# Performance work log

Measured on AMD Instinct MI355X. Metric: run time of the kernel, lower is better.

## Reference

```python
import jax, jax.numpy as jnp
import numpy as np

N = 131072; E = 1048576; B = 1024
FIN = 128; H = 128; K = 30; C1 = 16; KERN = 5
D = 3 * H                      # 384 = hidden*num_layers
POOL_LEN = (K - KERN + 1) // 2 # 13
EPS = 1e-5


def setup_inputs() -> dict:
    key = jax.random.key(0)
    ks = jax.random.split(key, 12)
    w = lambda k, shape, s=0.05: (jax.random.normal(k, shape, jnp.float32) * s)
    z = jax.random.randint(ks[0], (N,), 0, FIN, dtype=jnp.int32)
    edge_index = jax.random.randint(ks[1], (2, E), 0, N, dtype=jnp.int32)
    batch = jnp.sort(jax.random.randint(ks[2], (N,), 0, B, dtype=jnp.int32))
    return dict(
        z=z, edge_index=edge_index, batch=batch,
        W0=w(ks[3], (FIN, H)), b0=jnp.zeros((H,), jnp.float32),
        W1=w(ks[4], (H, H)),   b1=jnp.zeros((H,), jnp.float32),
        W2=w(ks[5], (H, H)),   b2=jnp.zeros((H,), jnp.float32),
        Wc1=w(ks[6], (C1, D)), bc1=jnp.zeros((C1,), jnp.float32),
        Wc2=w(ks[7], (2 * C1, C1, KERN)), bc2=jnp.zeros((2 * C1,), jnp.float32),
        g1=jnp.ones((C1,), jnp.float32),  be1=jnp.zeros((C1,), jnp.float32),
        g2=jnp.ones((2 * C1,), jnp.float32), be2=jnp.zeros((2 * C1,), jnp.float32),
        Wl1=w(ks[8], (128, 2 * C1 * POOL_LEN)), bl1=jnp.zeros((128,), jnp.float32),
        Wl2=w(ks[9], (1, 128)), bl2=jnp.zeros((1,), jnp.float32),
        rm1=jnp.zeros((C1,), jnp.float32), rv1=jnp.ones((C1,), jnp.float32),
        rm2=jnp.zeros((2 * C1,), jnp.float32), rv2=jnp.ones((2 * C1,), jnp.float32),
    )


def _bn(h, g, be, rm, rv):
    # eval-mode BatchNorm1d over channel axis 1 of [B, C, L]
    scale = (g * jax.lax.rsqrt(rv + EPS))[None, :, None]
    return (h - rm[None, :, None]) * scale + be[None, :, None]


def _forward(z, edge_index, batch, W0, b0, W1, b1, W2, b2, Wc1, bc1, Wc2, bc2,
             g1, be1, g2, be2, Wl1, bl1, Wl2, bl2, rm1, rv1, rm2, rv2):
    # --- GCN normalization with self-loops (PyG gcn_norm) ---
    loops = jnp.arange(N)
    row = jnp.concatenate([edge_index[0], loops])  # source
    col = jnp.concatenate([edge_index[1], loops])  # target (aggregation)
    deg = jax.ops.segment_sum(jnp.ones(E + N, jnp.float32), col, num_segments=N)
    dis = jax.lax.rsqrt(deg)  # deg >= 1 thanks to self-loops
    norm = dis[row] * dis[col]

    def gcn(x, W, b):
        msg = (x @ W)[row] * norm[:, None]              # [E+N, H]
        return jax.ops.segment_sum(msg, col, num_segments=N) + b

    x = jax.nn.one_hot(z, FIN, dtype=jnp.float32)       # [N, FIN]
    xs = []
    for W, b in ((W0, b0), (W1, b1), (W2, b2)):
        x = jnp.tanh(gcn(x, W, b))
        xs.append(x)
    x = jnp.concatenate(xs, axis=-1)                    # [N, D]

    # --- global_sort_pool: per graph, sort by last channel desc, keep top-k, zero-pad ---
    order = jnp.lexsort((-x[:, -1], batch))             # batch asc, last-channel desc
    xb, bs = x[order], batch[order]
    counts = jax.ops.segment_sum(jnp.ones(N, jnp.int32), batch, num_segments=B)
    starts = jnp.cumsum(counts) - counts
    rank = jnp.arange(N) - starts[bs]                   # within-graph rank
    dest = jnp.where(rank < K, rank, K)                 # overflow bucket at K
    pooled = jnp.zeros((B, K + 1, D), jnp.float32).at[bs, dest].set(xb)[:, :K]  # [B,K,D]

    # --- conv1d_1 (kernel=stride=D) == dense over the D channels of each kept node ---
    h = jnp.einsum('bkd,cd->bck', pooled, Wc1) + bc1[None, :, None]  # [B,C1,K]
    h = _bn(jax.nn.relu(h), g1, be1, rm1, rv1)
    # --- conv1d_2 ---
    h = jax.lax.conv_general_dilated(h, Wc2, (1,), 'VALID',
                                     dimension_numbers=('NCH', 'OIH', 'NCH'))
    h = h + bc2[None, :, None]                          # [B,2C1,K-KERN+1]
    h = _bn(jax.nn.relu(h), g2, be2, rm2, rv2)
    # --- maxpool(2,2), flatten, dense head (dropout is identity in eval) ---
    h = h.reshape(B, 2 * C1, POOL_LEN, 2).max(-1)
    h = jax.nn.relu(h.reshape(B, -1) @ Wl1.T + bl1)
    return (h @ Wl2.T + bl2).reshape(-1)                # [B]


def reference(z, edge_index, batch, W0, b0, W1, b1, W2, b2, Wc1, bc1, Wc2, bc2,
              g1, be1, g2, be2, Wl1, bl1, Wl2, bl2, rm1, rv1, rm2, rv2):
    return _forward(z, edge_index, batch, W0, b0, W1, b1, W2, b2, Wc1, bc1, Wc2, bc2,
                    g1, be1, g2, be2, Wl1, bl1, Wl2, bl2, rm1, rv1, rm2, rv2)
```

## Files before the change

### kernel.cpp

```cpp
#include <hip/hip_runtime.h>
#include <math.h>

constexpr int HD = 128;
constexpr int DD = 384;
constexpr int KK = 30;
constexpr int C1N = 16;
constexpr int C2N = 32;
constexpr int KERN5 = 5;
constexpr int CONVL = 26;
constexpr int PL = 13;
constexpr int FLAT = 416;

__global__ void deg_kernel(const int* __restrict__ col, int* __restrict__ cnt, int E) {
  int e = blockIdx.x * blockDim.x + threadIdx.x;
  if (e < E) atomicAdd(&cnt[col[e]], 1);
}

__global__ void scan1_kernel(const int* __restrict__ cnt, int* __restrict__ bsum, int N) {
  __shared__ int red[256];
  int t = threadIdx.x, b = blockIdx.x;
  int base = b * 1024 + t * 4;
  int s = 0;
#pragma unroll
  for (int j = 0; j < 4; ++j) { int idx = base + j; if (idx < N) s += cnt[idx]; }
  red[t] = s;
  __syncthreads();
  for (int o = 128; o > 0; o >>= 1) { if (t < o) red[t] += red[t + o]; __syncthreads(); }
  if (t == 0) bsum[b] = red[0];
}

__global__ void scan2_kernel(int* __restrict__ bsum, int nb) {
  __shared__ int s[1024];
  int t = threadIdx.x;
  int v = (t < nb) ? bsum[t] : 0;
  s[t] = v;
  __syncthreads();
  for (int o = 1; o < 1024; o <<= 1) {
    int u = (t >= o) ? s[t - o] : 0;
    __syncthreads();
    s[t] += u;
    __syncthreads();
  }
  if (t < nb) bsum[t] = s[t] - v;
}

__global__ void scan3_kernel(const int* __restrict__ cnt, const int* __restrict__ bsum,
                             int* __restrict__ offsets, float* __restrict__ dis, int N) {
  __shared__ int red[256];
  int t = threadIdx.x, b = blockIdx.x;
  int base = b * 1024 + t * 4;
  int v[4]; int s = 0;
#pragma unroll
  for (int j = 0; j < 4; ++j) { int idx = base + j; v[j] = (idx < N) ? cnt[idx] : 0; s += v[j]; }
  red[t] = s;
  __syncthreads();
  for (int o = 1; o < 256; o <<= 1) {
    int u = (t >= o) ? red[t - o] : 0;
    __syncthreads();
    red[t] += u;
    __syncthreads();
  }
  int run = bsum[b] + red[t] - s;
#pragma unroll
  for (int j = 0; j < 4; ++j) {
    int idx = base + j;
    if (idx < N) {
      offsets[idx] = run;
      run += v[j];
      dis[idx] = 1.0f / sqrtf((float)(v[j] + 1));
      if (idx == N - 1) offsets[N] = run;
    }
  }
}

__global__ void fill_kernel(const int* __restrict__ row, const int* __restrict__ col,
                            const int* __restrict__ offsets, int* __restrict__ cursor,
                            int* __restrict__ csr_src, int E) {
  int e = blockIdx.x * blockDim.x + threadIdx.x;
  if (e < E) {
    int c = col[e];
    int p = offsets[c] + atomicAdd(&cursor[c], 1);
    csr_src[p] = row[e];
  }
}

__global__ __launch_bounds__(256) void agg0_kernel(
    const int* __restrict__ z, const int* __restrict__ offsets,
    const int* __restrict__ csr_src, const float* __restrict__ dis,
    const float* __restrict__ W0, const float* __restrict__ b0,
    float* __restrict__ x1, int N) {
  int hw = (blockIdx.x * blockDim.x + threadIdx.x) >> 5;
  int lane = threadIdx.x & 31;
  if (hw >= N) return;
  int i = hw;
  int c0 = lane * 4;
  float di = dis[i];
  int beg = offsets[i], end = offsets[i + 1];
  float ax = 0.f, ay = 0.f, az = 0.f, aw = 0.f;
  int e = beg;
  for (; e + 8 <= end; e += 8) {
    int s0 = csr_src[e],     s1 = csr_src[e + 1], s2 = csr_src[e + 2], s3 = csr_src[e + 3];
    int s4 = csr_src[e + 4], s5 = csr_src[e + 5], s6 = csr_src[e + 6], s7 = csr_src[e + 7];
    float w0 = dis[s0], w1 = dis[s1], w2 = dis[s2], w3 = dis[s3];
    float w4 = dis[s4], w5 = dis[s5], w6 = dis[s6], w7 = dis[s7];
    const float4 y0 = *(const float4*)(W0 + (size_t)z[s0] * HD + c0);
    const float4 y1 = *(const float4*)(W0 + (size_t)z[s1] * HD + c0);
    const float4 y2 = *(const float4*)(W0 + (size_t)z[s2] * HD + c0);
    const float4 y3 = *(const float4*)(W0 + (size_t)z[s3] * HD + c0);
    const float4 y4 = *(const float4*)(W0 + (size_t)z[s4] * HD + c0);
    const float4 y5 = *(const float4*)(W0 + (size_t)z[s5] * HD + c0);
    const float4 y6 = *(const float4*)(W0 + (size_t)z[s6] * HD + c0);
    const float4 y7 = *(const float4*)(W0 + (size_t)z[s7] * HD + c0);
    ax = fmaf(w0, y0.x, fmaf(w1, y1.x, fmaf(w2, y2.x, fmaf(w3, y3.x, ax))));
    ay = fmaf(w0, y0.y, fmaf(w1, y1.y, fmaf(w2, y2.y, fmaf(w3, y3.y, ay))));
    az = fmaf(w0, y0.z, fmaf(w1, y1.z, fmaf(w2, y2.z, fmaf(w3, y3.z, az))));
    aw = fmaf(w0, y0.w, fmaf(w1, y1.w, fmaf(w2, y2.w, fmaf(w3, y3.w, aw))));
    ax = fmaf(w4, y4.x, fmaf(w5, y5.x, fmaf(w6, y6.x, fmaf(w7, y7.x, ax))));
    ay = fmaf(w4, y4.y, fmaf(w5, y5.y, fmaf(w6, y6.y, fmaf(w7, y7.y, ay))));
    az = fmaf(w4, y4.z, fmaf(w5, y5.z, fmaf(w6, y6.z, fmaf(w7, y7.z, az))));
    aw = fmaf(w4, y4.w, fmaf(w5, y5.w, fmaf(w6, y6.w, fmaf(w7, y7.w, aw))));
  }
  for (; e + 4 <= end; e += 4) {
    int s0 = csr_src[e], s1 = csr_src[e + 1], s2 = csr_src[e + 2], s3 = csr_src[e + 3];
    float w0 = dis[s0], w1 = dis[s1], w2 = dis[s2], w3 = dis[s3];
    const float4 y0 = *(const float4*)(W0 + (size_t)z[s0] * HD + c0);
    const float4 y1 = *(const float4*)(W0 + (size_t)z[s1] * HD + c0);
    const float4 y2 = *(const float4*)(W0 + (size_t)z[s2] * HD + c0);
    const float4 y3 = *(const float4*)(W0 + (size_t)z[s3] * HD + c0);
    ax = fmaf(w0, y0.x, fmaf(w1, y1.x, fmaf(w2, y2.x, fmaf(w3, y3.x, ax))));
    ay = fmaf(w0, y0.y, fmaf(w1, y1.y, fmaf(w2, y2.y, fmaf(w3, y3.y, ay))));
    az = fmaf(w0, y0.z, fmaf(w1, y1.z, fmaf(w2, y2.z, fmaf(w3, y3.z, az))));
    aw = fmaf(w0, y0.w, fmaf(w1, y1.w, fmaf(w2, y2.w, fmaf(w3, y3.w, aw))));
  }
  for (; e < end; ++e) {
    int s = csr_src[e];
    float w = dis[s];
    const float4 ys = *(const float4*)(W0 + (size_t)z[s] * HD + c0);
    ax = fmaf(w, ys.x, ax);
    ay = fmaf(w, ys.y, ay);
    az = fmaf(w, ys.z, az);
    aw = fmaf(w, ys.w, aw);
  }
  const float4 yi = *(const float4*)(W0 + (size_t)z[i] * HD + c0);
  const float4 bb = *(const float4*)(b0 + c0);
  float inv = di * di;
  float4 o = make_float4(tanhf(di * ax + inv * yi.x + bb.x),
                         tanhf(di * ay + inv * yi.y + bb.y),
                         tanhf(di * az + inv * yi.z + bb.z),
                         tanhf(di * aw + inv * yi.w + bb.w));
  *(float4*)(x1 + (size_t)i * HD + c0) = o;
}

__global__ __launch_bounds__(256) void agg_kernel(
    const float* __restrict__ x, const int* __restrict__ offsets,
    const int* __restrict__ csr_src, const float* __restrict__ dis,
    float* __restrict__ T, int N) {
  int hw = (blockIdx.x * blockDim.x + threadIdx.x) >> 5;
  int lane = threadIdx.x & 31;
  if (hw >= N) return;
  int i = hw;
  int c0 = lane * 4;
  float di = dis[i];
  int beg = offsets[i], end = offsets[i + 1];
  float ax = 0.f, ay = 0.f, az = 0.f, aw = 0.f;
  int e = beg;
  for (; e + 8 <= end; e += 8) {
    int s0 = csr_src[e],     s1 = csr_src[e + 1], s2 = csr_src[e + 2], s3 = csr_src[e + 3];
    int s4 = csr_src[e + 4], s5 = csr_src[e + 5], s6 = csr_src[e + 6], s7 = csr_src[e + 7];
    float w0 = dis[s0], w1 = dis[s1], w2 = dis[s2], w3 = dis[s3];
    float w4 = dis[s4], w5 = dis[s5], w6 = dis[s6], w7 = dis[s7];
    const float4 y0 = *(const float4*)(x + (size_t)s0 * HD + c0);
    const float4 y1 = *(const float4*)(x + (size_t)s1 * HD + c0);
    const float4 y2 = *(const float4*)(x + (size_t)s2 * HD + c0);
    const float4 y3 = *(const float4*)(x + (size_t)s3 * HD + c0);
    const float4 y4 = *(const float4*)(x + (size_t)s4 * HD + c0);
    const float4 y5 = *(const float4*)(x + (size_t)s5 * HD + c0);
    const float4 y6 = *(const float4*)(x + (size_t)s6 * HD + c0);
    const float4 y7 = *(const float4*)(x + (size_t)s7 * HD + c0);
    ax = fmaf(w0, y0.x, fmaf(w1, y1.x, fmaf(w2, y2.x, fmaf(w3, y3.x, ax))));
    ay = fmaf(w0, y0.y, fmaf(w1, y1.y, fmaf(w2, y2.y, fmaf(w3, y3.y, ay))));
    az = fmaf(w0, y0.z, fmaf(w1, y1.z, fmaf(w2, y2.z, fmaf(w3, y3.z, az))));
    aw = fmaf(w0, y0.w, fmaf(w1, y1.w, fmaf(w2, y2.w, fmaf(w3, y3.w, aw))));
    ax = fmaf(w4, y4.x, fmaf(w5, y5.x, fmaf(w6, y6.x, fmaf(w7, y7.x, ax))));
    ay = fmaf(w4, y4.y, fmaf(w5, y5.y, fmaf(w6, y6.y, fmaf(w7, y7.y, ay))));
    az = fmaf(w4, y4.z, fmaf(w5, y5.z, fmaf(w6, y6.z, fmaf(w7, y7.z, az))));
    aw = fmaf(w4, y4.w, fmaf(w5, y5.w, fmaf(w6, y6.w, fmaf(w7, y7.w, aw))));
  }
  for (; e + 4 <= end; e += 4) {
    int s0 = csr_src[e], s1 = csr_src[e + 1], s2 = csr_src[e + 2], s3 = csr_src[e + 3];
    float w0 = dis[s0], w1 = dis[s1], w2 = dis[s2], w3 = dis[s3];
    const float4 y0 = *(const float4*)(x + (size_t)s0 * HD + c0);
    const float4 y1 = *(const float4*)(x + (size_t)s1 * HD + c0);
    const float4 y2 = *(const float4*)(x + (size_t)s2 * HD + c0);
    const float4 y3 = *(const float4*)(x + (size_t)s3 * HD + c0);
    ax = fmaf(w0, y0.x, fmaf(w1, y1.x, fmaf(w2, y2.x, fmaf(w3, y3.x, ax))));
    ay = fmaf(w0, y0.y, fmaf(w1, y1.y, fmaf(w2, y2.y, fmaf(w3, y3.y, ay))));
    az = fmaf(w0, y0.z, fmaf(w1, y1.z, fmaf(w2, y2.z, fmaf(w3, y3.z, az))));
    aw = fmaf(w0, y0.w, fmaf(w1, y1.w, fmaf(w2, y2.w, fmaf(w3, y3.w, aw))));
  }
  for (; e < end; ++e) {
    int s = csr_src[e];
    float w = dis[s];
    const float4 ys = *(const float4*)(x + (size_t)s * HD + c0);
    ax = fmaf(w, ys.x, ax);
    ay = fmaf(w, ys.y, ay);
    az = fmaf(w, ys.z, az);
    aw = fmaf(w, ys.w, aw);
  }
  const float4 xi = *(const float4*)(x + (size_t)i * HD + c0);
  float inv = di * di;
  float4 o = make_float4(di * ax + inv * xi.x, di * ay + inv * xi.y,
                         di * az + inv * xi.z, di * aw + inv * xi.w);
  *(float4*)(T + (size_t)i * HD + c0) = o;
}

__global__ __launch_bounds__(512) void gemm_kernel(
    float* __restrict__ T, const float* __restrict__ W, const float* __restrict__ b, int N) {
  __shared__ float Xs[128][33];
  __shared__ float Ws[32][128];
  int t = threadIdx.x;
  int r0 = blockIdx.x * 128;
  int ty = t >> 4, tx = t & 15;
  int R0 = ty * 4;
  float acc[4][8];
#pragma unroll
  for (int a = 0; a < 4; ++a)
#pragma unroll
    for (int c = 0; c < 8; ++c) acc[a][c] = 0.f;

  for (int kb = 0; kb < 128; kb += 32) {
    __syncthreads();
    for (int l = t; l < 1024; l += 512) {
      int r = l >> 3, c4 = (l & 7) << 2;
      float4 v = *(const float4*)(T + (size_t)(r0 + r) * HD + kb + c4);
      Xs[r][c4] = v.x; Xs[r][c4 + 1] = v.y; Xs[r][c4 + 2] = v.z; Xs[r][c4 + 3] = v.w;
    }
    for (int l = t; l < 1024; l += 512) {
      int k = l >> 5, c4 = (l & 31) << 2;
      *(float4*)(&Ws[k][c4]) = *(const float4*)(W + (size_t)(kb + k) * HD + c4);
    }
    __syncthreads();
#pragma unroll
    for (int k = 0; k < 32; ++k) {
      float a[4];
#pragma unroll
      for (int ri = 0; ri < 4; ++ri) a[ri] = Xs[R0 + ri][k];
      float4 blo = *(const float4*)(&Ws[k][tx * 4]);
      float4 bhi = *(const float4*)(&Ws[k][64 + tx * 4]);
      float bb[8] = {blo.x, blo.y, blo.z, blo.w, bhi.x, bhi.y, bhi.z, bhi.w};
#pragma unroll
      for (int ri = 0; ri < 4; ++ri)
#pragma unroll
        for (int ci = 0; ci < 8; ++ci)
          acc[ri][ci] = fmaf(a[ri], bb[ci], acc[ri][ci]);
    }
  }
  float4 bl = *(const float4*)(b + tx * 4);
  float4 bh = *(const float4*)(b + 64 + tx * 4);
#pragma unroll
  for (int ri = 0; ri < 4; ++ri) {
    float4 o0 = make_float4(tanhf(acc[ri][0] + bl.x), tanhf(acc[ri][1] + bl.y),
                            tanhf(acc[ri][2] + bl.z), tanhf(acc[ri][3] + bl.w));
    float4 o1 = make_float4(tanhf(acc[ri][4] + bh.x), tanhf(acc[ri][5] + bh.y),
                            tanhf(acc[ri][6] + bh.z), tanhf(acc[ri][7] + bh.w));
    *(float4*)(T + (size_t)(r0 + R0 + ri) * HD + tx * 4) = o0;
    *(float4*)(T + (size_t)(r0 + R0 + ri) * HD + 64 + tx * 4) = o1;
  }
}

__global__ void gstart_kernel(const int* __restrict__ batch, int* __restrict__ gstart,
                              int N, int B) {
  int g = blockIdx.x * blockDim.x + threadIdx.x;
  if (g > B) return;
  int lo = 0, hi = N;
  while (lo < hi) { int mid = (lo + hi) >> 1; if (batch[mid] < g) lo = mid + 1; else hi = mid; }
  gstart[g] = lo;
}

__global__ __launch_bounds__(512) void head_kernel(
    const float* __restrict__ X1, const float* __restrict__ X2, const float* __restrict__ X3,
    const int* __restrict__ gstart,
    const float* __restrict__ Wc1, const float* __restrict__ bc1,
    const float* __restrict__ Wc2, const float* __restrict__ bc2,
    const float* __restrict__ g1, const float* __restrict__ be1,
    const float* __restrict__ g2, const float* __restrict__ be2,
    const float* __restrict__ rm1, const float* __restrict__ rv1,
    const float* __restrict__ rm2, const float* __restrict__ rv2,
    const float* __restrict__ Wl1, const float* __restrict__ bl1,
    const float* __restrict__ Wl2, const float* __restrict__ bl2,
    float* __restrict__ out) {
  constexpr int MAXC = 512;
  __shared__ float vals[MAXC];
  __shared__ int   sel[KK];
  __shared__ float ph[KK][385];
  __shared__ float h1b[C1N][KK + 1];
  float* h2b  = &ph[0][0];
  float* pp   = &ph[0][0] + 832;
  float* part = &ph[0][0] + 1248;
  float* l1v  = &ph[0][0] + 1760;

  int g = blockIdx.x, t = threadIdx.x;
  int start = gstart[g];
  int count = gstart[g + 1] - start;
  if (count > MAXC) count = MAXC;
  int kk = count < KK ? count : KK;

  for (int i = t; i < count; i += 512)
    vals[i] = X3[(size_t)(start + i) * HD + (HD - 1)];
  __syncthreads();
  if (t < count) {
    float vi = vals[t];
    int rank = 0;
    for (int j = 0; j < count; ++j) {
      float vj = vals[j];
      rank += (vj > vi) || (vj == vi && j < t);
    }
    if (rank < KK) sel[rank] = t;
  }
  __syncthreads();

  for (int l = t; l < KK * DD; l += 512) {
    int r = l / DD, d = l - r * DD;
    float v = 0.f;
    if (r < kk) {
      size_t n = (size_t)(start + sel[r]);
      v = (d < HD) ? X1[n * HD + d]
        : (d < 2 * HD) ? X2[n * HD + (d - HD)]
                       : X3[n * HD + (d - 2 * HD)];
    }
    ph[r][d] = v;
  }
  __syncthreads();

  if (t < C1N * KK) {
    int c = t / KK, k = t - c * KK;
    const float* w = Wc1 + c * DD;
    float s = bc1[c];
    for (int d = 0; d < DD; ++d) s = fmaf(ph[k][d], w[d], s);
    s = fmaxf(s, 0.f);
    float sc = g1[c] * rsqrtf(rv1[c] + 1e-5f);
    h1b[c][k] = (s - rm1[c]) * sc + be1[c];
  }
  __syncthreads();

  for (int l = t; l < C2N * CONVL; l += 512) {
    int o = l / CONVL, tt = l - o * CONVL;
    float s = bc2[o];
    const float* w = Wc2 + o * (C1N * KERN5);
#pragma unroll
    for (int c = 0; c < C1N; ++c)
#pragma unroll
      for (int q = 0; q < KERN5; ++q)
        s = fmaf(h1b[c][tt + q], w[c * KERN5 + q], s);
    s = fmaxf(s, 0.f);
    float sc = g2[o] * rsqrtf(rv2[o] + 1e-5f);
    h2b[o * CONVL + tt] = (s - rm2[o]) * sc + be2[o];
  }
  __syncthreads();

  if (t < FLAT) {
    int o = t / PL, u = t - o * PL;
    pp[t] = fmaxf(h2b[o * CONVL + 2 * u], h2b[o * CONVL + 2 * u + 1]);
  }
  __syncthreads();

  {
    int j = t & 127, h = t >> 7;
    const int Q = FLAT / 4;
    const float* w = Wl1 + (size_t)j * FLAT + h * Q;
    float s = (h == 0) ? bl1[j] : 0.f;
    for (int f = 0; f < Q; ++f) s = fmaf(pp[h * Q + f], w[f], s);
    part[t] = s;
  }
  __syncthreads();
  if (t < 128) l1v[t] = fmaxf(part[t] + part[t + 128] + part[t + 256] + part[t + 384], 0.f);
  __syncthreads();

  if (t < 64) {
    float s = l1v[t] * Wl2[t] + l1v[t + 64] * Wl2[t + 64];
#pragma unroll
    for (int o2 = 32; o2 > 0; o2 >>= 1) s += __shfl_down(s, o2);
    if (t == 0) out[g] = s + bl2[0];
  }
}

extern "C" void kernel_launch(void* const* d_in, const int* in_sizes, int n_in,
                              void* d_out, int out_size, void* d_ws, size_t ws_size,
                              hipStream_t stream) {
  const int*   z    = (const int*)d_in[0];
  const int*   ei   = (const int*)d_in[1];
  const int*   batch= (const int*)d_in[2];
  const float* W0   = (const float*)d_in[3];
  const float* b0   = (const float*)d_in[4];
  const float* W1   = (const float*)d_in[5];
  const float* b1   = (const float*)d_in[6];
  const float* W2   = (const float*)d_in[7];
  const float* b2   = (const float*)d_in[8];
  const float* Wc1  = (const float*)d_in[9];
  const float* bc1  = (const float*)d_in[10];
  const float* Wc2  = (const float*)d_in[11];
  const float* bc2  = (const float*)d_in[12];
  const float* g1   = (const float*)d_in[13];
  const float* be1  = (const float*)d_in[14];
  const float* g2   = (const float*)d_in[15];
  const float* be2  = (const float*)d_in[16];
  const float* Wl1  = (const float*)d_in[17];
  const float* bl1  = (const float*)d_in[18];
  const float* Wl2  = (const float*)d_in[19];
  const float* bl2  = (const float*)d_in[20];
  const float* rm1  = (const float*)d_in[21];
  const float* rv1  = (const float*)d_in[22];
  const float* rm2  = (const float*)d_in[23];
  const float* rv2  = (const float*)d_in[24];

  const int N = in_sizes[0];
  const int E = in_sizes[1] / 2;
  const int B = out_size;
  const int* rowp = ei;
  const int* colp = ei + E;

  char* base = (char*)d_ws;
  size_t off = 0;
  auto alloc = [&](size_t bytes) -> void* {
    void* p = base + off;
    off += (bytes + 255) & ~(size_t)255;
    return p;
  };
  int*   cnt     = (int*)alloc((size_t)N * 4);
  int*   offsets = (int*)alloc(((size_t)N + 1) * 4);
  int*   cursor  = (int*)alloc((size_t)N * 4);
  int*   csr_src = (int*)alloc((size_t)E * 4);
  float* dis     = (float*)alloc((size_t)N * 4);
  int*   gstart  = (int*)alloc(((size_t)B + 1) * 4);
  int*   bsum    = (int*)alloc(1024 * 4);
  float* X1      = (float*)alloc((size_t)N * HD * 4);
  float* X2      = (float*)alloc((size_t)N * HD * 4);
  float* X3      = (float*)alloc((size_t)N * HD * 4);
  (void)ws_size; (void)n_in;

  hipMemsetAsync(cnt, 0, (size_t)N * 4, stream);
  hipMemsetAsync(cursor, 0, (size_t)N * 4, stream);

  const int nb = (N + 1023) / 1024;
  deg_kernel<<<(E + 255) / 256, 256, 0, stream>>>(colp, cnt, E);
  scan1_kernel<<<nb, 256, 0, stream>>>(cnt, bsum, N);
  scan2_kernel<<<1, 1024, 0, stream>>>(bsum, nb);
  scan3_kernel<<<nb, 256, 0, stream>>>(cnt, bsum, offsets, dis, N);
  fill_kernel<<<(E + 255) / 256, 256, 0, stream>>>(rowp, colp, offsets, cursor, csr_src, E);

  agg0_kernel<<<N / 8, 256, 0, stream>>>(z, offsets, csr_src, dis, W0, b0, X1, N);
  agg_kernel<<<N / 8, 256, 0, stream>>>(X1, offsets, csr_src, dis, X2, N);
  gemm_kernel<<<N / 128, 512, 0, stream>>>(X2, W1, b1, N);
  agg_kernel<<<N / 8, 256, 0, stream>>>(X2, offsets, csr_src, dis, X3, N);
  gemm_kernel<<<N / 128, 512, 0, stream>>>(X3, W2, b2, N);

  gstart_kernel<<<(B + 1 + 255) / 256, 256, 0, stream>>>(batch, gstart, N, B);
  head_kernel<<<B, 512, 0, stream>>>(X1, X2, X3, gstart, Wc1, bc1, Wc2, bc2, g1, be1, g2, be2,
                                     rm1, rv1, rm2, rv2, Wl1, bl1, Wl2, bl2, (float*)d_out);
}
```

Measured before the change: 684.6 us.

## Replace FP32 SIMT GEMM with bf16x3 split MFMA GEMM

Replaces the scalar-FMA 128x128 dense layers with a matrix-core kernel. Activations are split on the fly into three bf16 parts and weights are pre-split and transposed once per call, then combined with six bf16 MFMA products to approximate FP32 accuracy. This targets the FP32 ALU cost of the two dense layers, at the price of extra split arithmetic and LDS traffic. Weight fragments are read straight from global memory, and output stores are scalar and strided.

```diff
diff --git a/kernel.cpp b/kernel.cpp
--- a/kernel.cpp
+++ b/kernel.cpp
@@ -11,6 +11,9 @@
 constexpr int PL = 13;
 constexpr int FLAT = 416;
 
+typedef __attribute__((ext_vector_type(8))) short bf16x8;
+typedef __attribute__((ext_vector_type(4))) float f32x4;
+
 __global__ void deg_kernel(const int* __restrict__ col, int* __restrict__ cnt, int E) {
   int e = blockIdx.x * blockDim.x + threadIdx.x;
   if (e < E) atomicAdd(&cnt[col[e]], 1);
@@ -82,6 +85,27 @@
     int p = offsets[c] + atomicAdd(&cursor[c], 1);
     csr_src[p] = row[e];
   }
+}
+
+__device__ __forceinline__ ushort bf16_rne(float x) {
+  uint32_t bits = __float_as_uint(x);
+  uint32_t r = bits + 0x7FFFu + ((bits >> 16) & 1u);
+  return (ushort)(r >> 16);
+}
+
+__global__ void wprep_kernel(const float* __restrict__ W, ushort* __restrict__ WhT,
+                             ushort* __restrict__ WmT, ushort* __restrict__ WlT) {
+  int t = blockIdx.x * 256 + threadIdx.x;
+  int k = t >> 7, col = t & 127;
+  float x = W[k * 128 + col];
+  ushort h = bf16_rne(x);
+  float r1 = x - __uint_as_float(((uint32_t)h) << 16);
+  ushort m = bf16_rne(r1);
+  float r2 = r1 - __uint_as_float(((uint32_t)m) << 16);
+  ushort l = bf16_rne(r2);
+  WhT[col * 128 + k] = h;
+  WmT[col * 128 + k] = m;
+  WlT[col * 128 + k] = l;
 }
 
 __global__ __launch_bounds__(256) void agg0_kernel(
@@ -214,57 +238,79 @@
   *(float4*)(T + (size_t)i * HD + c0) = o;
 }
 
-__global__ __launch_bounds__(512) void gemm_kernel(
-    float* __restrict__ T, const float* __restrict__ W, const float* __restrict__ b, int N) {
-  __shared__ float Xs[128][33];
-  __shared__ float Ws[32][128];
+__global__ __launch_bounds__(512) void gemm_mfma_kernel(
+    float* __restrict__ T, const ushort* __restrict__ WhT, const ushort* __restrict__ WmT,
+    const ushort* __restrict__ WlT, const float* __restrict__ b, int N) {
+  __shared__ ushort Ah[128][40];
+  __shared__ ushort Am[128][40];
+  __shared__ ushort Al[128][40];
   int t = threadIdx.x;
   int r0 = blockIdx.x * 128;
-  int ty = t >> 4, tx = t & 15;
-  int R0 = ty * 4;
-  float acc[4][8];
-#pragma unroll
-  for (int a = 0; a < 4; ++a)
-#pragma unroll
-    for (int c = 0; c < 8; ++c) acc[a][c] = 0.f;
-
-  for (int kb = 0; kb < 128; kb += 32) {
+  int w = t >> 6, l = t & 63;
+  int lr = l & 15, lg = l >> 4;
+  f32x4 acc[8];
+#pragma unroll
+  for (int n = 0; n < 8; ++n) acc[n] = (f32x4){0.f, 0.f, 0.f, 0.f};
+
+  for (int kb = 0; kb < 4; ++kb) {
     __syncthreads();
-    for (int l = t; l < 1024; l += 512) {
-      int r = l >> 3, c4 = (l & 7) << 2;
-      float4 v = *(const float4*)(T + (size_t)(r0 + r) * HD + kb + c4);
-      Xs[r][c4] = v.x; Xs[r][c4 + 1] = v.y; Xs[r][c4 + 2] = v.z; Xs[r][c4 + 3] = v.w;
-    }
-    for (int l = t; l < 1024; l += 512) {
-      int k = l >> 5, c4 = (l & 31) << 2;
-      *(float4*)(&Ws[k][c4]) = *(const float4*)(W + (size_t)(kb + k) * HD + c4);
+    {
+      int r = t >> 2, c8 = (t & 3) * 8;
+      const float* src = T + (size_t)(r0 + r) * HD + kb * 32 + c8;
+      float4 v0 = *(const float4*)src;
+      float4 v1 = *(const float4*)(src + 4);
+      float xs[8] = {v0.x, v0.y, v0.z, v0.w, v1.x, v1.y, v1.z, v1.w};
+      uint32_t hp[4], mp[4], lp[4];
+#pragma unroll
+      for (int j = 0; j < 4; ++j) {
+        ushort h0 = bf16_rne(xs[2 * j]);
+        ushort h1 = bf16_rne(xs[2 * j + 1]);
+        float r10 = xs[2 * j]     - __uint_as_float(((uint32_t)h0) << 16);
+        float r11 = xs[2 * j + 1] - __uint_as_float(((uint32_t)h1) << 16);
+        ushort m0 = bf16_rne(r10);
+        ushort m1 = bf16_rne(r11);
+        float r20 = r10 - __uint_as_float(((uint32_t)m0) << 16);
+        float r21 = r11 - __uint_as_float(((uint32_t)m1) << 16);
+        ushort l0 = bf16_rne(r20);
+        ushort l1 = bf16_rne(r21);
+        hp[j] = (uint32_t)h0 | ((uint32_t)h1 << 16);
+        mp[j] = (uint32_t)m0 | ((uint32_t)m1 << 16);
+        lp[j] = (uint32_t)l0 | ((uint32_t)l1 << 16);
+      }
+      uint32_t* ah = (uint32_t*)&Ah[r][c8];
+      uint32_t* am = (uint32_t*)&Am[r][c8];
+      uint32_t* al = (uint32_t*)&Al[r][c8];
+#pragma unroll
+      for (int j = 0; j < 4; ++j) { ah[j] = hp[j]; am[j] = mp[j]; al[j] = lp[j]; }
     }
     __syncthreads();
-#pragma unroll
-    for (int k = 0; k < 32; ++k) {
-      float a[4];
-#pragma unroll
-      for (int ri = 0; ri < 4; ++ri) a[ri] = Xs[R0 + ri][k];
-      float4 blo = *(const float4*)(&Ws[k][tx * 4]);
-      float4 bhi = *(const float4*)(&Ws[k][64 + tx * 4]);
-      float bb[8] = {blo.x, blo.y, blo.z, blo.w, bhi.x, bhi.y, bhi.z, bhi.w};
-#pragma unroll
-      for (int ri = 0; ri < 4; ++ri)
-#pragma unroll
-        for (int ci = 0; ci < 8; ++ci)
-          acc[ri][ci] = fmaf(a[ri], bb[ci], acc[ri][ci]);
+
+    bf16x8 fa_h = *(const bf16x8*)(&Ah[16 * w + lr][8 * lg]);
+    bf16x8 fa_m = *(const bf16x8*)(&Am[16 * w + lr][8 * lg]);
+    bf16x8 fa_l = *(const bf16x8*)(&Al[16 * w + lr][8 * lg]);
+    int kk = kb * 32 + 8 * lg;
+#pragma unroll
+    for (int n = 0; n < 8; ++n) {
+      bf16x8 fb_h = *(const bf16x8*)(WhT + (size_t)(16 * n + lr) * 128 + kk);
+      bf16x8 fb_m = *(const bf16x8*)(WmT + (size_t)(16 * n + lr) * 128 + kk);
+      bf16x8 fb_l = *(const bf16x8*)(WlT + (size_t)(16 * n + lr) * 128 + kk);
+      acc[n] = __builtin_amdgcn_mfma_f32_16x16x32_bf16(fa_h, fb_h, acc[n], 0, 0, 0);
+      acc[n] = __builtin_amdgcn_mfma_f32_16x16x32_bf16(fa_h, fb_m, acc[n], 0, 0, 0);
+      acc[n] = __builtin_amdgcn_mfma_f32_16x16x32_bf16(fa_m, fb_h, acc[n], 0, 0, 0);
+      acc[n] = __builtin_amdgcn_mfma_f32_16x16x32_bf16(fa_h, fb_l, acc[n], 0, 0, 0);
+      acc[n] = __builtin_amdgcn_mfma_f32_16x16x32_bf16(fa_m, fb_m, acc[n], 0, 0, 0);
+      acc[n] = __builtin_amdgcn_mfma_f32_16x16x32_bf16(fa_l, fb_h, acc[n], 0, 0, 0);
     }
   }
-  float4 bl = *(const float4*)(b + tx * 4);
-  float4 bh = *(const float4*)(b + 64 + tx * 4);
-#pragma unroll
-  for (int ri = 0; ri < 4; ++ri) {
-    float4 o0 = make_float4(tanhf(acc[ri][0] + bl.x), tanhf(acc[ri][1] + bl.y),
-                            tanhf(acc[ri][2] + bl.z), tanhf(acc[ri][3] + bl.w));
-    float4 o1 = make_float4(tanhf(acc[ri][4] + bh.x), tanhf(acc[ri][5] + bh.y),
-                            tanhf(acc[ri][6] + bh.z), tanhf(acc[ri][7] + bh.w));
-    *(float4*)(T + (size_t)(r0 + R0 + ri) * HD + tx * 4) = o0;
-    *(float4*)(T + (size_t)(r0 + R0 + ri) * HD + 64 + tx * 4) = o1;
+
+#pragma unroll
+  for (int n = 0; n < 8; ++n) {
+    float bc = b[16 * n + lr];
+#pragma unroll
+    for (int r = 0; r < 4; ++r) {
+      int row = r0 + 16 * w + 4 * lg + r;
+      T[(size_t)row * HD + 16 * n + lr] = tanhf(acc[n][r] + bc);
+    }
   }
 }
 
@@ -426,16 +472,22 @@
     off += (bytes + 255) & ~(size_t)255;
     return p;
   };
-  int*   cnt     = (int*)alloc((size_t)N * 4);
-  int*   offsets = (int*)alloc(((size_t)N + 1) * 4);
-  int*   cursor  = (int*)alloc((size_t)N * 4);
-  int*   csr_src = (int*)alloc((size_t)E * 4);
-  float* dis     = (float*)alloc((size_t)N * 4);
-  int*   gstart  = (int*)alloc(((size_t)B + 1) * 4);
-  int*   bsum    = (int*)alloc(1024 * 4);
-  float* X1      = (float*)alloc((size_t)N * HD * 4);
-  float* X2      = (float*)alloc((size_t)N * HD * 4);
-  float* X3      = (float*)alloc((size_t)N * HD * 4);
+  int*    cnt     = (int*)alloc((size_t)N * 4);
+  int*    offsets = (int*)alloc(((size_t)N + 1) * 4);
+  int*    cursor  = (int*)alloc((size_t)N * 4);
+  int*    csr_src = (int*)alloc((size_t)E * 4);
+  float*  dis     = (float*)alloc((size_t)N * 4);
+  int*    gstart  = (int*)alloc(((size_t)B + 1) * 4);
+  int*    bsum    = (int*)alloc(1024 * 4);
+  ushort* WhT1    = (ushort*)alloc(128 * 128 * 2);
+  ushort* WmT1    = (ushort*)alloc(128 * 128 * 2);
+  ushort* WlT1    = (ushort*)alloc(128 * 128 * 2);
+  ushort* WhT2    = (ushort*)alloc(128 * 128 * 2);
+  ushort* WmT2    = (ushort*)alloc(128 * 128 * 2);
+  ushort* WlT2    = (ushort*)alloc(128 * 128 * 2);
+  float*  X1      = (float*)alloc((size_t)N * HD * 4);
+  float*  X2      = (float*)alloc((size_t)N * HD * 4);
+  float*  X3      = (float*)alloc((size_t)N * HD * 4);
   (void)ws_size; (void)n_in;
 
   hipMemsetAsync(cnt, 0, (size_t)N * 4, stream);
@@ -447,12 +499,14 @@
   scan2_kernel<<<1, 1024, 0, stream>>>(bsum, nb);
   scan3_kernel<<<nb, 256, 0, stream>>>(cnt, bsum, offsets, dis, N);
   fill_kernel<<<(E + 255) / 256, 256, 0, stream>>>(rowp, colp, offsets, cursor, csr_src, E);
+  wprep_kernel<<<64, 256, 0, stream>>>(W1, WhT1, WmT1, WlT1);
+  wprep_kernel<<<64, 256, 0, stream>>>(W2, WhT2, WmT2, WlT2);
 
   agg0_kernel<<<N / 8, 256, 0, stream>>>(z, offsets, csr_src, dis, W0, b0, X1, N);
   agg_kernel<<<N / 8, 256, 0, stream>>>(X1, offsets, csr_src, dis, X2, N);
-  gemm_kernel<<<N / 128, 512, 0, stream>>>(X2, W1, b1, N);
+  gemm_mfma_kernel<<<N / 128, 512, 0, stream>>>(X2, WhT1, WmT1, WlT1, b1, N);
   agg_kernel<<<N / 8, 256, 0, stream>>>(X2, offsets, csr_src, dis, X3, N);
-  gemm_kernel<<<N / 128, 512, 0, stream>>>(X3, W2, b2, N);
+  gemm_mfma_kernel<<<N / 128, 512, 0, stream>>>(X3, WhT2, WmT2, WlT2, b2, N);
 
   gstart_kernel<<<(B + 1 + 255) / 256, 256, 0, stream>>>(batch, gstart, N, B);
   head_kernel<<<B, 512, 0, stream>>>(X1, X2, X3, gstart, Wc1, bc1, Wc2, bc2, g1, be1, g2, be2,
```

Result: slower. 773.0 us (+12.9%).
